# Kernel optimization log

Measured on AMD Instinct MI355X. Metric: run time of the kernel, lower is better.

Reference implementation:

```python
import jax, jax.numpy as jnp
import numpy as np

EMBED = 512
HEADS = 8
HEAD_DIM = EMBED // HEADS
N, T = 512, 64


def setup_inputs() -> dict:
    key = jax.random.key(0)
    ks = jax.random.split(key, 11)
    s = 1.0 / np.sqrt(EMBED)
    inp = {
        'values': jax.random.normal(ks[0], (N, T, EMBED), jnp.float32),
        'keys':   jax.random.normal(ks[1], (N, T, EMBED), jnp.float32),
        'query':  jax.random.normal(ks[2], (N, T, EMBED), jnp.float32),
        'Wv': jax.random.uniform(ks[3], (EMBED, EMBED), jnp.float32, -s, s),
        'bv': jax.random.uniform(ks[4], (EMBED,), jnp.float32, -s, s),
        'Wk': jax.random.uniform(ks[5], (EMBED, EMBED), jnp.float32, -s, s),
        'bk': jax.random.uniform(ks[6], (EMBED,), jnp.float32, -s, s),
        'Wq': jax.random.uniform(ks[7], (EMBED, EMBED), jnp.float32, -s, s),
        'bq': jax.random.uniform(ks[8], (EMBED,), jnp.float32, -s, s),
        'Wo': jax.random.uniform(ks[9], (EMBED, EMBED), jnp.float32, -s, s),
        'bo': jax.random.uniform(ks[10], (EMBED,), jnp.float32, -s, s),
    }
    return inp


def reference(values, keys, query, Wv, bv, Wk, bk, Wq, bq, Wo, bo):
    n, t, c = query.shape
    v = (values @ Wv.T + bv).reshape(n, t, HEADS, HEAD_DIM)
    k = (keys   @ Wk.T + bk).reshape(n, t, HEADS, HEAD_DIM)
    q = (query  @ Wq.T + bq).reshape(n, t, HEADS, HEAD_DIM)
    # attention over the batch axis: energy[q,k,t,h]
    energy = jnp.einsum('qthd,kthd->qkth', q, k)
    attn = jax.nn.softmax(energy / jnp.sqrt(jnp.float32(EMBED)), axis=1)
    out = jnp.einsum('qkth,kthd->qthd', attn, v).reshape(n, t, HEADS * HEAD_DIM)
    return out @ Wo.T + bo
```

## Files before the change

### kernel.cpp

```cpp
#include <hip/hip_runtime.h>
#include <hip/hip_bf16.h>
#include <math.h>

#define NBATCH 512
#define TT 64
#define EMB 512
#define NHEADS 8
#define HDIM 64
#define MROWS (NBATCH * TT)
#define ROWSTRIDE (TT * EMB)
#define WSEG 262144

static constexpr float QSCALE = 0.0637587140f;

typedef __attribute__((ext_vector_type(8))) short short8v;
typedef __attribute__((ext_vector_type(4))) float f32x4;

__device__ __forceinline__ unsigned short f2bf(float x) {
    union { float f; unsigned int u; } v; v.f = x;
    unsigned int r = v.u + 0x7fff + ((v.u >> 16) & 1);
    return (unsigned short)(r >> 16);
}

__device__ __forceinline__ unsigned int cvtpk(float lo, float hi) {
    unsigned int r;
    asm("v_cvt_pk_bf16_f32 %0, %1, %2" : "=v"(r) : "v"(lo), "v"(hi));
    return r;
}

__device__ __forceinline__ void gl16(const void* g, void* l) {
    __builtin_amdgcn_global_load_lds(
        (const __attribute__((address_space(1))) unsigned int*)g,
        (__attribute__((address_space(3))) unsigned int*)l, 16, 0, 0);
}

__global__ __launch_bounds__(256) void cvtw(
    const float* __restrict__ w0, const float* __restrict__ w1,
    const float* __restrict__ w2, const float* __restrict__ w3,
    unsigned short* __restrict__ dst)
{
    const int seg = blockIdx.y;
    const float* src = (seg == 0) ? w0 : (seg == 1) ? w1 : (seg == 2) ? w2 : w3;
    const float sc = (seg == 0) ? QSCALE : 1.0f;
    const size_t i = (size_t)blockIdx.x * 256 + threadIdx.x;
    float4 v = reinterpret_cast<const float4*>(src)[i];
    ushort4 r;
    r.x = f2bf(v.x * sc); r.y = f2bf(v.y * sc); r.z = f2bf(v.z * sc); r.w = f2bf(v.w * sc);
    reinterpret_cast<ushort4*>(dst + (size_t)seg * WSEG)[i] = r;
}

__global__ __launch_bounds__(512) void gemm_proj3(
    const float* __restrict__ A0, const float* __restrict__ A1,
    const float* __restrict__ A2, const unsigned short* __restrict__ Wb,
    const float* __restrict__ b0, const float* __restrict__ b1, const float* __restrict__ b2,
    unsigned short* __restrict__ o0, unsigned short* __restrict__ o1, unsigned short* __restrict__ o2)
{
    __shared__ __align__(16) float Asf[2][128 * 32];
    __shared__ __align__(16) unsigned short Bs[2][512 * 32];
    const int z = blockIdx.y;
    const float* A = (z == 0) ? A0 : (z == 1) ? A1 : A2;
    const unsigned short* W = Wb + (size_t)z * WSEG;
    const float* bias = (z == 0) ? b0 : (z == 1) ? b1 : b2;
    const float bsc = (z == 0) ? QSCALE : 1.0f;
    unsigned short* Cout = (z == 0) ? o0 : (z == 1) ? o1 : o2;

    const int tid = threadIdx.x;
    const int wave = tid >> 6, lane = tid & 63;
    const int lg = lane >> 4, li = lane & 15;
    const int m0 = blockIdx.x * 128;
    const int wm = (wave >> 2) * 64;
    const int wn = (wave & 3) * 128;

    f32x4 acc[4][8] = {};

    const int au = (tid & 7) ^ ((tid >> 3) & 7);
    const float* gaf = A + (size_t)(m0 + (tid >> 3)) * 512 + au * 4;
    const unsigned short* gb = W + (size_t)(tid >> 2) * 512 + (tid & 3) * 8;

#define ISSUE(t, bb) do {                                                   \
        const int _k0 = (t) * 32;                                           \
        gl16(gaf + _k0, &Asf[bb][wave * 256]);                              \
        gl16(gaf + _k0 + (size_t)64 * 512, &Asf[bb][wave * 256 + 2048]);    \
        _Pragma("unroll")                                                   \
        for (int _i = 0; _i < 4; _i++)                                      \
            gl16(gb + _k0 + (size_t)_i * 128 * 512,                         \
                 &Bs[bb][wave * 512 + _i * 4096]);                          \
    } while (0)

    ISSUE(0, 0);
    ISSUE(1, 1);

    for (int t = 0; t < 16; ++t) {
        if (t < 15) { asm volatile("s_waitcnt vmcnt(6)" ::: "memory"); }
        else        { asm volatile("s_waitcnt vmcnt(0)" ::: "memory"); }
        __builtin_amdgcn_s_barrier();
        __builtin_amdgcn_sched_barrier(0);

        const int b = t & 1;
        short8v af[4];
#pragma unroll
        for (int i = 0; i < 4; i++) {
            const int r = wm + i * 16 + li;
            const int rx = li & 7;
            const float4 fa = *reinterpret_cast<const float4*>(
                &Asf[b][r * 32 + ((lg * 2) ^ rx) * 4]);
            const float4 fb = *reinterpret_cast<const float4*>(
                &Asf[b][r * 32 + ((lg * 2 + 1) ^ rx) * 4]);
            union { unsigned int u[4]; short8v v; } pk;
            pk.u[0] = cvtpk(fa.x, fa.y); pk.u[1] = cvtpk(fa.z, fa.w);
            pk.u[2] = cvtpk(fb.x, fb.y); pk.u[3] = cvtpk(fb.z, fb.w);
            af[i] = pk.v;
        }
#pragma unroll
        for (int j = 0; j < 8; j++) {
            const short8v bfr = *reinterpret_cast<const short8v*>(
                &Bs[b][(wn + j * 16 + li) * 32 + lg * 8]);
#pragma unroll
            for (int i = 0; i < 4; i++)
                acc[i][j] = __builtin_amdgcn_mfma_f32_16x16x32_bf16(af[i], bfr, acc[i][j], 0, 0, 0);
        }

        asm volatile("s_waitcnt lgkmcnt(0)" ::: "memory");
        __builtin_amdgcn_s_barrier();
        __builtin_amdgcn_sched_barrier(0);
        if (t + 2 < 16) ISSUE(t + 2, b);
    }
#undef ISSUE

#pragma unroll
    for (int j = 0; j < 8; j++) {
        const int col = wn + j * 16 + li;
        const float bb = bias[col] * bsc;
#pragma unroll
        for (int i = 0; i < 4; i++) {
            const int row0 = m0 + wm + i * 16 + lg * 4;
#pragma unroll
            for (int r = 0; r < 4; r++)
                Cout[(size_t)(row0 + r) * 512 + col] = f2bf(acc[i][j][r] + bb);
        }
    }
}

__global__ __launch_bounds__(256) void gemm_out(
    const unsigned short* __restrict__ A, const unsigned short* __restrict__ W,
    const float* __restrict__ bias, float* __restrict__ Cout)
{
    __shared__ __align__(16) unsigned short As[128 * 32];
    __shared__ __align__(16) unsigned short Bs[128 * 32];
    const int tid = threadIdx.x;
    const int wave = tid >> 6, lane = tid & 63;
    const int lg = lane >> 4, li = lane & 15;
    const int m0 = blockIdx.x * 128;
    const int n0 = blockIdx.y * 128;
    const int wr = (wave >> 1) * 64;
    const int wc = (wave & 1) * 64;

    f32x4 acc[4][4] = {};

    const unsigned short* ga = A + (size_t)(m0 + (tid >> 2)) * 512 + (tid & 3) * 8;
    const unsigned short* gb = W + (size_t)(n0 + (tid >> 2)) * 512 + (tid & 3) * 8;
    unsigned short* lA = &As[wave * 512];
    unsigned short* lB = &Bs[wave * 512];

    for (int k0 = 0; k0 < 512; k0 += 32) {
        __syncthreads();
        gl16(ga + k0, lA);
        gl16(ga + k0 + 64 * 512, lA + 2048);
        gl16(gb + k0, lB);
        gl16(gb + k0 + 64 * 512, lB + 2048);
        __syncthreads();

        short8v af[4], bfr[4];
#pragma unroll
        for (int i = 0; i < 4; i++) {
            af[i]  = *reinterpret_cast<const short8v*>(&As[(wr + i * 16 + li) * 32 + lg * 8]);
            bfr[i] = *reinterpret_cast<const short8v*>(&Bs[(wc + i * 16 + li) * 32 + lg * 8]);
        }
#pragma unroll
        for (int i = 0; i < 4; i++)
#pragma unroll
            for (int j = 0; j < 4; j++)
                acc[i][j] = __builtin_amdgcn_mfma_f32_16x16x32_bf16(af[i], bfr[j], acc[i][j], 0, 0, 0);
    }

#pragma unroll
    for (int j = 0; j < 4; j++) {
        const int col = n0 + wc + j * 16 + li;
        const float bb = bias[col];
#pragma unroll
        for (int i = 0; i < 4; i++) {
            const int row0 = m0 + wr + i * 16 + lg * 4;
#pragma unroll
            for (int r = 0; r < 4; r++)
                Cout[(size_t)(row0 + r) * 512 + col] = acc[i][j][r] + bb;
        }
    }
}

__global__ __launch_bounds__(256) void attn_bf16(
    const unsigned short* __restrict__ qp, const unsigned short* __restrict__ kp,
    const unsigned short* __restrict__ vp, unsigned short* __restrict__ ao)
{
    __shared__ __align__(16) unsigned short Ks[64 * 64];
    __shared__ __align__(16) unsigned short Vt[64][68];
    __shared__ __align__(16) unsigned short Pl[4][16][72];

    const int tid = threadIdx.x;
    const int wave = tid >> 6, lane = tid & 63;
    const int lg = lane >> 4, li = lane & 15;
    const int n0 = blockIdx.x * 256;
    const int th = blockIdx.y;
    const size_t base = (size_t)(th >> 3) * EMB + (size_t)(th & 7) * HDIM;

    short8v qf[4][2];
#pragma unroll
    for (int mf = 0; mf < 4; mf++)
#pragma unroll
        for (int kf = 0; kf < 2; kf++)
            qf[mf][kf] = *reinterpret_cast<const short8v*>(
                qp + (size_t)(n0 + wave * 64 + mf * 16 + li) * ROWSTRIDE
                   + base + kf * 32 + lg * 8);

    const int vd0 = (tid & 15) * 4;
    const int vk0 = (tid >> 4) * 4;
    const unsigned short* gv = vp + base + vd0;
    uint2 vl[4];
#pragma unroll
    for (int i = 0; i < 4; i++)
        vl[i] = *reinterpret_cast<const uint2*>(gv + (size_t)(vk0 + i) * ROWSTRIDE);

    const short8v ones = (short8v)(short)0x3F80;
    f32x4 acc[4][4] = {};
    f32x4 acc_l[4] = {};

    for (int kv = 0; kv < 8; kv++) {
        const int k0 = kv * 64;
        __syncthreads();

        {
            unsigned short* lk = &Ks[wave * 512];
#pragma unroll
            for (int i = 0; i < 2; i++) {
                const int r = (tid >> 3) + i * 32;
                const int srcofs = (((tid & 7) * 8) ^ ((r & 7) * 8));
                gl16(kp + (size_t)(k0 + r) * ROWSTRIDE + base + srcofs, lk + i * 2048);
            }
        }
#pragma unroll
        for (int dd = 0; dd < 4; dd++) {
            const unsigned int sel = (dd & 1) ? 0x07060302u : 0x05040100u;
            const unsigned int a = (dd < 2) ? vl[0].x : vl[0].y;
            const unsigned int b = (dd < 2) ? vl[1].x : vl[1].y;
            const unsigned int c = (dd < 2) ? vl[2].x : vl[2].y;
            const unsigned int d = (dd < 2) ? vl[3].x : vl[3].y;
            uint2 o;
            o.x = __builtin_amdgcn_perm(b, a, sel);
            o.y = __builtin_amdgcn_perm(d, c, sel);
            *reinterpret_cast<uint2*>(&Vt[vd0 + dd][vk0]) = o;
        }
        __syncthreads();

        if (kv < 7) {
#pragma unroll
            for (int i = 0; i < 4; i++)
                vl[i] = *reinterpret_cast<const uint2*>(
                    gv + (size_t)(k0 + 64 + vk0 + i) * ROWSTRIDE);
        }

        short8v kfr[4][2], vfr[4][2];
#pragma unroll
        for (int nf = 0; nf < 4; nf++) {
            const int key = nf * 16 + li;
#pragma unroll
            for (int kf = 0; kf < 2; kf++)
                kfr[nf][kf] = *reinterpret_cast<const short8v*>(
                    &Ks[key * 64 + ((kf * 32 + lg * 8) ^ ((key & 7) * 8))]);
        }
#pragma unroll
        for (int df = 0; df < 4; df++)
#pragma unroll
            for (int kf = 0; kf < 2; kf++)
                vfr[df][kf] = *reinterpret_cast<const short8v*>(
                    &Vt[df * 16 + li][kf * 32 + lg * 8]);

#pragma unroll
        for (int mf = 0; mf < 4; mf++) {
            f32x4 s[4] = {};
#pragma unroll
            for (int nf = 0; nf < 4; nf++)
#pragma unroll
                for (int kf = 0; kf < 2; kf++)
                    s[nf] = __builtin_amdgcn_mfma_f32_16x16x32_bf16(kfr[nf][kf], qf[mf][kf], s[nf], 0, 0, 0);

#pragma unroll
            for (int nf = 0; nf < 4; nf++) {
                const float p0 = exp2f(s[nf][0]);
                const float p1 = exp2f(s[nf][1]);
                const float p2 = exp2f(s[nf][2]);
                const float p3 = exp2f(s[nf][3]);
                union { unsigned int u[2]; uint2 v; } pk2;
                pk2.u[0] = cvtpk(p0, p1);
                pk2.u[1] = cvtpk(p2, p3);
                *reinterpret_cast<uint2*>(&Pl[wave][li][nf * 16 + lg * 4]) = pk2.v;
            }

            short8v pf[2];
#pragma unroll
            for (int kf = 0; kf < 2; kf++)
                pf[kf] = *reinterpret_cast<const short8v*>(
                    &Pl[wave][li][kf * 32 + lg * 8]);
#pragma unroll
            for (int kf = 0; kf < 2; kf++)
                acc_l[mf] = __builtin_amdgcn_mfma_f32_16x16x32_bf16(pf[kf], ones, acc_l[mf], 0, 0, 0);
#pragma unroll
            for (int df = 0; df < 4; df++)
#pragma unroll
                for (int kf = 0; kf < 2; kf++)
                    acc[mf][df] = __builtin_amdgcn_mfma_f32_16x16x32_bf16(pf[kf], vfr[df][kf], acc[mf][df], 0, 0, 0);
        }
    }

#pragma unroll
    for (int mf = 0; mf < 4; mf++) {
#pragma unroll
        for (int r = 0; r < 4; r++) {
            const float linv = 1.0f / acc_l[mf][r];
            const int qrow = n0 + wave * 64 + mf * 16 + lg * 4 + r;
#pragma unroll
            for (int df = 0; df < 4; df++)
                ao[(size_t)qrow * ROWSTRIDE + base + df * 16 + li] = f2bf(acc[mf][df][r] * linv);
        }
    }
}

extern "C" void kernel_launch(void* const* d_in, const int* in_sizes, int n_in,
                              void* d_out, int out_size, void* d_ws, size_t ws_size,
                              hipStream_t stream) {
    const float* values = (const float*)d_in[0];
    const float* keys   = (const float*)d_in[1];
    const float* query  = (const float*)d_in[2];
    const float* Wv = (const float*)d_in[3];
    const float* bv = (const float*)d_in[4];
    const float* Wk = (const float*)d_in[5];
    const float* bk = (const float*)d_in[6];
    const float* Wq = (const float*)d_in[7];
    const float* bq = (const float*)d_in[8];
    const float* Wo = (const float*)d_in[9];
    const float* bo = (const float*)d_in[10];
    float* out = (float*)d_out;

    unsigned short* ws16 = (unsigned short*)d_ws;
    const size_t PLANE = (size_t)MROWS * EMB;
    unsigned short* qb = ws16;
    unsigned short* kb = ws16 + PLANE;
    unsigned short* vb = ws16 + 2 * PLANE;
    unsigned short* ab = ws16 + 3 * PLANE;
    unsigned short* wb = ws16 + 4 * PLANE;

    cvtw<<<dim3(WSEG / 4 / 256, 4), 256, 0, stream>>>(Wq, Wk, Wv, Wo, wb);

    gemm_proj3<<<dim3(MROWS / 128, 3), 512, 0, stream>>>(
        query, keys, values, wb, bq, bk, bv, qb, kb, vb);

    attn_bf16<<<dim3(2, TT * NHEADS), 256, 0, stream>>>(qb, kb, vb, ab);

    gemm_out<<<dim3(MROWS / 128, EMB / 128), 256, 0, stream>>>(
        ab, wb + 3 * WSEG, bo, out);
}
```

Before: 232.1 us.

## Pre-convert activations to bf16 and retile projection GEMM to 256x256 blocks

A new kernel converts query, keys and values to bf16 in workspace before the projection GEMM. The GEMM then loads bf16 A tiles directly, so it no longer converts fp32 to bf16 in registers, and uses 256x256 output tiles with a BK=64 XOR-swizzled LDS layout over a 3D grid. It also raises wave priority around the MFMA block and sets launch bounds to 2 blocks per CU. In exchange, the added conversion pass reads and writes the full activations once more, and each A row block is now read by two column tiles.

```diff
diff --git a/kernel.cpp b/kernel.cpp
--- a/kernel.cpp
+++ b/kernel.cpp
@@ -34,6 +34,23 @@
         (__attribute__((address_space(3))) unsigned int*)l, 16, 0, 0);
 }
 
+__global__ __launch_bounds__(256) void cvt3(
+    const float* __restrict__ a, const float* __restrict__ b, const float* __restrict__ c,
+    unsigned short* __restrict__ oa, unsigned short* __restrict__ ob, unsigned short* __restrict__ oc)
+{
+    const size_t i = (size_t)blockIdx.x * 256 + threadIdx.x;
+    float4 va = reinterpret_cast<const float4*>(a)[i];
+    float4 vb = reinterpret_cast<const float4*>(b)[i];
+    float4 vc = reinterpret_cast<const float4*>(c)[i];
+    ushort4 ra, rb, rc;
+    ra.x = f2bf(va.x); ra.y = f2bf(va.y); ra.z = f2bf(va.z); ra.w = f2bf(va.w);
+    rb.x = f2bf(vb.x); rb.y = f2bf(vb.y); rb.z = f2bf(vb.z); rb.w = f2bf(vb.w);
+    rc.x = f2bf(vc.x); rc.y = f2bf(vc.y); rc.z = f2bf(vc.z); rc.w = f2bf(vc.w);
+    reinterpret_cast<ushort4*>(oa)[i] = ra;
+    reinterpret_cast<ushort4*>(ob)[i] = rb;
+    reinterpret_cast<ushort4*>(oc)[i] = rc;
+}
+
 __global__ __launch_bounds__(256) void cvtw(
     const float* __restrict__ w0, const float* __restrict__ w1,
     const float* __restrict__ w2, const float* __restrict__ w3,
@@ -49,16 +66,16 @@
     reinterpret_cast<ushort4*>(dst + (size_t)seg * WSEG)[i] = r;
 }
 
-__global__ __launch_bounds__(512) void gemm_proj3(
-    const float* __restrict__ A0, const float* __restrict__ A1,
-    const float* __restrict__ A2, const unsigned short* __restrict__ Wb,
+__global__ __launch_bounds__(512, 2) void gemm_proj3(
+    const unsigned short* __restrict__ A0, const unsigned short* __restrict__ A1,
+    const unsigned short* __restrict__ A2, const unsigned short* __restrict__ Wb,
     const float* __restrict__ b0, const float* __restrict__ b1, const float* __restrict__ b2,
     unsigned short* __restrict__ o0, unsigned short* __restrict__ o1, unsigned short* __restrict__ o2)
 {
-    __shared__ __align__(16) float Asf[2][128 * 32];
-    __shared__ __align__(16) unsigned short Bs[2][512 * 32];
-    const int z = blockIdx.y;
-    const float* A = (z == 0) ? A0 : (z == 1) ? A1 : A2;
+    __shared__ __align__(16) unsigned short Asb[2][256 * 64];
+    __shared__ __align__(16) unsigned short Bsb[2][256 * 64];
+    const int z = blockIdx.z;
+    const unsigned short* A = (z == 0) ? A0 : (z == 1) ? A1 : A2;
     const unsigned short* W = Wb + (size_t)z * WSEG;
     const float* bias = (z == 0) ? b0 : (z == 1) ? b1 : b2;
     const float bsc = (z == 0) ? QSCALE : 1.0f;
@@ -67,76 +84,78 @@
     const int tid = threadIdx.x;
     const int wave = tid >> 6, lane = tid & 63;
     const int lg = lane >> 4, li = lane & 15;
-    const int m0 = blockIdx.x * 128;
-    const int wm = (wave >> 2) * 64;
-    const int wn = (wave & 3) * 128;
-
-    f32x4 acc[4][8] = {};
+    const int m0 = blockIdx.x * 256;
+    const int n0 = blockIdx.y * 256;
+    const int wm = (wave >> 2) * 128;
+    const int wn = (wave & 3) * 64;
+
+    f32x4 acc[8][4] = {};
 
     const int au = (tid & 7) ^ ((tid >> 3) & 7);
-    const float* gaf = A + (size_t)(m0 + (tid >> 3)) * 512 + au * 4;
-    const unsigned short* gb = W + (size_t)(tid >> 2) * 512 + (tid & 3) * 8;
+    const unsigned short* gA = A + (size_t)(m0 + (tid >> 3)) * 512 + au * 8;
+    const unsigned short* gW = W + (size_t)(n0 + (tid >> 3)) * 512 + au * 8;
 
 #define ISSUE(t, bb) do {                                                   \
-        const int _k0 = (t) * 32;                                           \
-        gl16(gaf + _k0, &Asf[bb][wave * 256]);                              \
-        gl16(gaf + _k0 + (size_t)64 * 512, &Asf[bb][wave * 256 + 2048]);    \
+        const int _k0 = (t) * 64;                                           \
         _Pragma("unroll")                                                   \
-        for (int _i = 0; _i < 4; _i++)                                      \
-            gl16(gb + _k0 + (size_t)_i * 128 * 512,                         \
-                 &Bs[bb][wave * 512 + _i * 4096]);                          \
+        for (int _i = 0; _i < 4; _i++) {                                    \
+            gl16(gA + _k0 + (size_t)_i * 64 * 512,                          \
+                 &Asb[bb][wave * 512 + _i * 4096]);                         \
+            gl16(gW + _k0 + (size_t)_i * 64 * 512,                          \
+                 &Bsb[bb][wave * 512 + _i * 4096]);                         \
+        }                                                                   \
     } while (0)
 
     ISSUE(0, 0);
     ISSUE(1, 1);
 
-    for (int t = 0; t < 16; ++t) {
-        if (t < 15) { asm volatile("s_waitcnt vmcnt(6)" ::: "memory"); }
-        else        { asm volatile("s_waitcnt vmcnt(0)" ::: "memory"); }
+    for (int t = 0; t < 8; ++t) {
+        if (t < 7) { asm volatile("s_waitcnt vmcnt(8)" ::: "memory"); }
+        else       { asm volatile("s_waitcnt vmcnt(0)" ::: "memory"); }
         __builtin_amdgcn_s_barrier();
         __builtin_amdgcn_sched_barrier(0);
 
         const int b = t & 1;
-        short8v af[4];
-#pragma unroll
-        for (int i = 0; i < 4; i++) {
-            const int r = wm + i * 16 + li;
-            const int rx = li & 7;
-            const float4 fa = *reinterpret_cast<const float4*>(
-                &Asf[b][r * 32 + ((lg * 2) ^ rx) * 4]);
-            const float4 fb = *reinterpret_cast<const float4*>(
-                &Asf[b][r * 32 + ((lg * 2 + 1) ^ rx) * 4]);
-            union { unsigned int u[4]; short8v v; } pk;
-            pk.u[0] = cvtpk(fa.x, fa.y); pk.u[1] = cvtpk(fa.z, fa.w);
-            pk.u[2] = cvtpk(fb.x, fb.y); pk.u[3] = cvtpk(fb.z, fb.w);
-            af[i] = pk.v;
-        }
-#pragma unroll
-        for (int j = 0; j < 8; j++) {
-            const short8v bfr = *reinterpret_cast<const short8v*>(
-                &Bs[b][(wn + j * 16 + li) * 32 + lg * 8]);
-#pragma unroll
-            for (int i = 0; i < 4; i++)
-                acc[i][j] = __builtin_amdgcn_mfma_f32_16x16x32_bf16(af[i], bfr, acc[i][j], 0, 0, 0);
-        }
+        __builtin_amdgcn_s_setprio(1);
+#pragma unroll
+        for (int kf = 0; kf < 2; kf++) {
+            const int xofs = (kf * 32 + lg * 8);
+            short8v bfr[4];
+#pragma unroll
+            for (int nf = 0; nf < 4; nf++) {
+                const int rB = wn + nf * 16 + li;
+                bfr[nf] = *reinterpret_cast<const short8v*>(
+                    &Bsb[b][rB * 64 + (xofs ^ ((rB & 7) * 8))]);
+            }
+#pragma unroll
+            for (int mf = 0; mf < 8; mf++) {
+                const int rA = wm + mf * 16 + li;
+                const short8v af = *reinterpret_cast<const short8v*>(
+                    &Asb[b][rA * 64 + (xofs ^ ((rA & 7) * 8))]);
+#pragma unroll
+                for (int nf = 0; nf < 4; nf++)
+                    acc[mf][nf] = __builtin_amdgcn_mfma_f32_16x16x32_bf16(af, bfr[nf], acc[mf][nf], 0, 0, 0);
+            }
+        }
+        __builtin_amdgcn_s_setprio(0);
 
         asm volatile("s_waitcnt lgkmcnt(0)" ::: "memory");
         __builtin_amdgcn_s_barrier();
         __builtin_amdgcn_sched_barrier(0);
-        if (t + 2 < 16) ISSUE(t + 2, b);
+        if (t + 2 < 8) ISSUE(t + 2, b);
     }
 #undef ISSUE
 
 #pragma unroll
-    for (int j = 0; j < 8; j++) {
-        const int col = wn + j * 16 + li;
+    for (int nf = 0; nf < 4; nf++) {
+        const int col = n0 + wn + nf * 16 + li;
         const float bb = bias[col] * bsc;
 #pragma unroll
-        for (int i = 0; i < 4; i++) {
-            const int row0 = m0 + wm + i * 16 + lg * 4;
+        for (int mf = 0; mf < 8; mf++) {
+            const int row0 = m0 + wm + mf * 16 + lg * 4;
 #pragma unroll
             for (int r = 0; r < 4; r++)
-                Cout[(size_t)(row0 + r) * 512 + col] = f2bf(acc[i][j][r] + bb);
+                Cout[(size_t)(row0 + r) * 512 + col] = f2bf(acc[mf][nf][r] + bb);
         }
     }
 }
@@ -351,16 +370,20 @@
 
     unsigned short* ws16 = (unsigned short*)d_ws;
     const size_t PLANE = (size_t)MROWS * EMB;
-    unsigned short* qb = ws16;
-    unsigned short* kb = ws16 + PLANE;
-    unsigned short* vb = ws16 + 2 * PLANE;
-    unsigned short* ab = ws16 + 3 * PLANE;
-    unsigned short* wb = ws16 + 4 * PLANE;
-
+    unsigned short* xq = ws16;
+    unsigned short* xk = ws16 + PLANE;
+    unsigned short* xv = ws16 + 2 * PLANE;
+    unsigned short* qb = ws16 + 3 * PLANE;
+    unsigned short* kb = ws16 + 4 * PLANE;
+    unsigned short* vb = ws16 + 5 * PLANE;
+    unsigned short* ab = ws16 + 6 * PLANE;
+    unsigned short* wb = ws16 + 7 * PLANE;
+
+    cvt3<<<PLANE / 4 / 256, 256, 0, stream>>>(query, keys, values, xq, xk, xv);
     cvtw<<<dim3(WSEG / 4 / 256, 4), 256, 0, stream>>>(Wq, Wk, Wv, Wo, wb);
 
-    gemm_proj3<<<dim3(MROWS / 128, 3), 512, 0, stream>>>(
-        query, keys, values, wb, bq, bk, bv, qb, kb, vb);
+    gemm_proj3<<<dim3(MROWS / 256, EMB / 256, 3), 512, 0, stream>>>(
+        xq, xk, xv, wb, bq, bk, bv, qb, kb, vb);
 
     attn_bf16<<<dim3(2, TT * NHEADS), 256, 0, stream>>>(qb, kb, vb, ab);
 
```

Result: slower. 244.0 us (+5.1%).
